# Kernel optimization log

Hardware: AMD Instinct MI355X
Metric: run time of the kernel (lower is better)

## Reference

```python
import jax, jax.numpy as jnp
import numpy as np

BATCH = 16
MAX_SEQLEN = 8192
D_MODEL = 1024
TOTAL = 65536  # sum of sequence lengths


def setup_inputs() -> dict:
    key = jax.random.key(0)
    k_buf, _ = jax.random.split(key)
    # Position buffer (e.g. precomputed position embeddings), first dim >= max length.
    buffer = jax.random.normal(k_buf, (MAX_SEQLEN, D_MODEL), dtype=jnp.float32)
    # Build ragged offsets: BATCH lengths, each <= MAX_SEQLEN, summing to TOTAL.
    rng = np.random.default_rng(0)
    base = TOTAL // BATCH  # 4096
    d = rng.integers(0, 2048, size=BATCH // 2)
    lengths = np.concatenate([base + d, base - d])
    rng.shuffle(lengths)
    offsets = jnp.asarray(np.concatenate([[0], np.cumsum(lengths)]), dtype=jnp.int32)
    return {"buffer": buffer, "offsets": offsets, "total_tokens": TOTAL}


def reference(buffer, offsets, total_tokens):
    # Equivalent of: for each sequence i with length L_i = offsets[i+1]-offsets[i],
    # take buffer[:L_i]; concatenate into jagged values sharing the same offsets.
    # Done in one vectorized pass: local position of each flat token = idx - offsets[seg].
    idx = jnp.arange(total_tokens, dtype=jnp.int32)                      # [T]
    seg = jnp.searchsorted(offsets, idx, side="right") - 1              # [T] sequence id
    pos = idx - offsets[seg]                                             # [T] ragged arange
    values = buffer[pos]                                                 # [T, D] jagged values
    return values
```

## Files before the change

### kernel.cpp

```cpp
#include <hip/hip_runtime.h>


#define D_MODEL 1024
#define VEC4_PER_ROW (D_MODEL / 4)
#define MAX_OFFSETS 64

__global__ __launch_bounds__(256) void positionid_gather(
    const float4* __restrict__ buf,
    const int*    __restrict__ offsets,
    int n_off,
    float4*       __restrict__ out)
{
    const int t = blockIdx.x;

    int seg = 0;
    #pragma unroll 4
    for (int i = 1; i < n_off - 1; ++i) {
        if (offsets[i] <= t) seg = i;
    }
    const int pos = t - offsets[seg];

    out[(size_t)t * VEC4_PER_ROW + threadIdx.x] =
        buf[(size_t)pos * VEC4_PER_ROW + threadIdx.x];
}

extern "C" void kernel_launch(void* const* d_in, const int* in_sizes, int n_in,
                              void* d_out, int out_size, void* d_ws, size_t ws_size,
                              hipStream_t stream) {
    const float4* buf     = (const float4*)d_in[0];
    const int*    offsets = (const int*)d_in[1];
    const int     n_off   = in_sizes[1];
    float4*       out     = (float4*)d_out;

    const int T = out_size / D_MODEL;

    positionid_gather<<<dim3(T), dim3(256), 0, stream>>>(buf, offsets, n_off, out);
}
```

Measured before the change: 305.5 us.

## Process 32 rows per block with shared offsets and nontemporal stores

Each block now copies 32 output rows instead of one. The offsets are staged once in shared memory and the segment is walked forward incrementally rather than searched again for every row. Loads are batched four at a time for more memory-level parallelism, and stores use nontemporal hints so the streaming output does not pollute the cache. There is no bounds check on T, so it assumes T is a multiple of 32, and the grid of 2048 blocks is smaller than before.

```diff
diff --git a/kernel.cpp b/kernel.cpp
--- a/kernel.cpp
+++ b/kernel.cpp
@@ -2,37 +2,63 @@
 
 
 #define D_MODEL 1024
-#define VEC4_PER_ROW (D_MODEL / 4)
-#define MAX_OFFSETS 64
+#define V4_PER_ROW (D_MODEL / 4)
+#define ROWS_PER_BLOCK 32
+#define THREADS 256
+#define MAX_OFF 64
 
-__global__ __launch_bounds__(256) void positionid_gather(
-    const float4* __restrict__ buf,
-    const int*    __restrict__ offsets,
+typedef float f32x4 __attribute__((ext_vector_type(4)));
+
+__global__ __launch_bounds__(THREADS) void positionid_gather(
+    const f32x4* __restrict__ buf,
+    const int*   __restrict__ offsets,
     int n_off,
-    float4*       __restrict__ out)
+    f32x4*       __restrict__ out,
+    int T)
 {
-    const int t = blockIdx.x;
+    __shared__ int s_off[MAX_OFF];
+    if (threadIdx.x < n_off) s_off[threadIdx.x] = offsets[threadIdx.x];
+    __syncthreads();
+
+    const int r0  = blockIdx.x * ROWS_PER_BLOCK;
+    const int tid = threadIdx.x;
 
     int seg = 0;
-    #pragma unroll 4
-    for (int i = 1; i < n_off - 1; ++i) {
-        if (offsets[i] <= t) seg = i;
+    for (int i = 1; i < n_off - 1; ++i)
+        if (s_off[i] <= r0) seg = i;
+    int nxt = s_off[seg + 1];
+
+    #pragma unroll
+    for (int rb = 0; rb < ROWS_PER_BLOCK; rb += 4) {
+        int pos[4];
+        #pragma unroll
+        for (int j = 0; j < 4; ++j) {
+            int t = r0 + rb + j;
+            while (t >= nxt && seg < n_off - 2) { ++seg; nxt = s_off[seg + 1]; }
+            pos[j] = t - s_off[seg];
+        }
+        f32x4 v[4];
+        #pragma unroll
+        for (int j = 0; j < 4; ++j)
+            v[j] = buf[(size_t)pos[j] * V4_PER_ROW + tid];
+        #pragma unroll
+        for (int j = 0; j < 4; ++j) {
+            int t = r0 + rb + j;
+            __builtin_nontemporal_store(v[j], &out[(size_t)t * V4_PER_ROW + tid]);
+        }
     }
-    const int pos = t - offsets[seg];
-
-    out[(size_t)t * VEC4_PER_ROW + threadIdx.x] =
-        buf[(size_t)pos * VEC4_PER_ROW + threadIdx.x];
 }
 
 extern "C" void kernel_launch(void* const* d_in, const int* in_sizes, int n_in,
                               void* d_out, int out_size, void* d_ws, size_t ws_size,
                               hipStream_t stream) {
-    const float4* buf     = (const float4*)d_in[0];
-    const int*    offsets = (const int*)d_in[1];
-    const int     n_off   = in_sizes[1];
-    float4*       out     = (float4*)d_out;
+    const f32x4* buf     = (const f32x4*)d_in[0];
+    const int*   offsets = (const int*)d_in[1];
+    const int    n_off   = in_sizes[1];
+    f32x4*       out     = (f32x4*)d_out;
 
     const int T = out_size / D_MODEL;
+    const int grid = (T + ROWS_PER_BLOCK - 1) / ROWS_PER_BLOCK;
 
-    positionid_gather<<<dim3(T), dim3(256), 0, stream>>>(buf, offsets, n_off, out);
+    positionid_gather<<<dim3(grid), dim3(THREADS), 0, stream>>>(buf, offsets, n_off, out, T);
 }
```

Measured after the change: 310.3 us. About the same (+1.6%).
